# Kernel optimization log

Hardware: AMD Instinct MI355X
Metric: run time of the kernel (lower is better)

## Reference

```python
import jax, jax.numpy as jnp
import numpy as np

L, B, D = 2048, 8, 1024
EPS = 1e-5


def setup_inputs() -> dict:
    key = jax.random.key(0)
    k1, k2 = jax.random.split(key)
    x = jax.random.normal(k1, (L, B, D), dtype=jnp.float32)
    c = jnp.zeros((B, D), dtype=jnp.float32)
    # w_ufr: Linear(D, 3D); weight init normal(std=0.001), bias zero except
    # the reset-gate third which is filled with 2.0 (per the torch init).
    W = jax.random.normal(k2, (3 * D, D), dtype=jnp.float32) * 0.001
    b = jnp.zeros((3 * D,), dtype=jnp.float32).at[2 * D:].set(2.0)
    gamma = jnp.ones((D,), dtype=jnp.float32)
    beta = jnp.zeros((D,), dtype=jnp.float32)
    return {"x": x, "c": c, "W": W, "b": b, "gamma": gamma, "beta": beta}


def _layernorm(x, gamma, beta):
    mu = jnp.mean(x, axis=-1, keepdims=True)
    var = jnp.var(x, axis=-1, keepdims=True)
    return (x - mu) * jax.lax.rsqrt(var + EPS) * gamma + beta


def reference(x, c, W, b, gamma, beta):
    residual = x
    x_norm = _layernorm(x, gamma, beta)            # [L,B,D]
    ufr = jnp.einsum('lbd,ed->lbe', x_norm, W) + b  # [L,B,3D]
    u, f, r = jnp.split(ufr, 3, axis=-1)
    f_gate = jax.nn.sigmoid(f)
    r_gate = jax.nn.sigmoid(r)

    def step(c_prev, fu):
        f_t, u_t = fu
        c_t = f_t * c_prev + (1.0 - f_t) * u_t
        return c_t, c_t

    last_c, c_stack = jax.lax.scan(step, c, (f_gate, u))  # c_stack: [L,B,D]
    hs = r_gate * jnp.tanh(c_stack) + (1.0 - r_gate) * x_norm
    # dropout is identity in eval mode
    return residual + hs, last_c
```

## Files before the change

### kernel.cpp

```cpp
#include <hip/hip_runtime.h>
#include <hip/hip_bf16.h>

#define L_DIM 2048
#define B_DIM 8
#define D_DIM 1024
#define M_DIM (L_DIM * B_DIM)
#define N_DIM (3 * D_DIM)
#define K_DIM D_DIM
#define BD (B_DIM * D_DIM)
#define NCHUNK 64
#define CLEN (L_DIM / NCHUNK)

typedef __attribute__((ext_vector_type(8))) __bf16 bf16x8;
typedef __attribute__((ext_vector_type(4))) __bf16 bf16x4;
typedef __attribute__((ext_vector_type(4))) float f32x4;

#define GLOAD_LDS16(g, l)                                        \
  __builtin_amdgcn_global_load_lds(                              \
      (const __attribute__((address_space(1))) void*)(g),        \
      (__attribute__((address_space(3))) void*)(l), 16, 0, 0)

__device__ __forceinline__ float sigmoidf_(float v) {
  return 1.0f / (1.0f + __expf(-v));
}

__global__ __launch_bounds__(256) void ln_kernel(
    const float* __restrict__ x, const float* __restrict__ gamma,
    const float* __restrict__ beta, __bf16* __restrict__ xn) {
  const int row = blockIdx.x;
  const int tid = threadIdx.x;
  const float4 v = ((const float4*)(x + (size_t)row * D_DIM))[tid];
  float s  = v.x + v.y + v.z + v.w;
  float ss = v.x * v.x + v.y * v.y + v.z * v.z + v.w * v.w;
  #pragma unroll
  for (int off = 32; off > 0; off >>= 1) {
    s  += __shfl_xor(s, off);
    ss += __shfl_xor(ss, off);
  }
  __shared__ float sb[8];
  const int wid = tid >> 6, lane = tid & 63;
  if (lane == 0) { sb[wid] = s; sb[4 + wid] = ss; }
  __syncthreads();
  const float tot  = sb[0] + sb[1] + sb[2] + sb[3];
  const float tot2 = sb[4] + sb[5] + sb[6] + sb[7];
  const float mu  = tot * (1.0f / D_DIM);
  const float var = tot2 * (1.0f / D_DIM) - mu * mu;
  const float rstd = rsqrtf(var + 1e-5f);
  const float4 g  = ((const float4*)gamma)[tid];
  const float4 bt = ((const float4*)beta)[tid];
  bf16x4 o;
  o[0] = (__bf16)((v.x - mu) * rstd * g.x + bt.x);
  o[1] = (__bf16)((v.y - mu) * rstd * g.y + bt.y);
  o[2] = (__bf16)((v.z - mu) * rstd * g.z + bt.z);
  o[3] = (__bf16)((v.w - mu) * rstd * g.w + bt.w);
  ((bf16x4*)(xn + (size_t)row * D_DIM))[tid] = o;
}

__global__ __launch_bounds__(256) void wconv_kernel(
    const float* __restrict__ W, __bf16* __restrict__ Wb) {
  const size_t i = ((size_t)blockIdx.x * 256 + threadIdx.x) * 4;
  const float4 v = *(const float4*)(W + i);
  bf16x4 o;
  o[0] = (__bf16)v.x; o[1] = (__bf16)v.y; o[2] = (__bf16)v.z; o[3] = (__bf16)v.w;
  *(bf16x4*)(Wb + i) = o;
}

__global__ __launch_bounds__(256) void gemm_kernel(
    const __bf16* __restrict__ A,
    const __bf16* __restrict__ Bm,
    const float* __restrict__ bias,
    __bf16* __restrict__ U, __bf16* __restrict__ FG, __bf16* __restrict__ RG) {
  __shared__ __bf16 As[128 * 64];
  __shared__ __bf16 Bs[128 * 64];
  const int tid = threadIdx.x;
  const int lane = tid & 63;
  const int wid = tid >> 6;
  const int wm = wid >> 1, wn = wid & 1;
  const int bm = blockIdx.x, bn = blockIdx.y;

  f32x4 acc[4][4] = {};

  const __bf16* Agbase = A + (size_t)(bm * 128) * K_DIM;
  const __bf16* Bgbase = Bm + (size_t)(bn * 128) * K_DIM;

  for (int kt = 0; kt < K_DIM / 64; ++kt) {
    __syncthreads();
    #pragma unroll
    for (int it = 0; it < 4; ++it) {
      const int ci = it * 256 + tid;
      const int row = ci >> 3, c8 = ci & 7;
      const size_t goff = (size_t)row * K_DIM + kt * 64 + c8 * 8;
      GLOAD_LDS16(Agbase + goff, As + (size_t)ci * 8);
      GLOAD_LDS16(Bgbase + goff, Bs + (size_t)ci * 8);
    }
    __syncthreads();
    #pragma unroll
    for (int ks = 0; ks < 2; ++ks) {
      const int kof = ks * 32 + (lane >> 4) * 8;
      bf16x8 af[4], bf[4];
      #pragma unroll
      for (int fm = 0; fm < 4; ++fm) {
        const int r = wm * 64 + fm * 16 + (lane & 15);
        af[fm] = *(const bf16x8*)(As + r * 64 + kof);
      }
      #pragma unroll
      for (int fn = 0; fn < 4; ++fn) {
        const int r = wn * 64 + fn * 16 + (lane & 15);
        bf[fn] = *(const bf16x8*)(Bs + r * 64 + kof);
      }
      #pragma unroll
      for (int fm = 0; fm < 4; ++fm)
        #pragma unroll
        for (int fn = 0; fn < 4; ++fn)
          acc[fm][fn] = __builtin_amdgcn_mfma_f32_16x16x32_bf16(
              af[fm], bf[fn], acc[fm][fn], 0, 0, 0);
    }
  }

  const int seg = (bn * 128) >> 10;
  const int nbase = (bn * 128) & 1023;
  __bf16* outb = (seg == 0) ? U : ((seg == 1) ? FG : RG);
  const int ccol = lane & 15;
  const int crow = (lane >> 4) * 4;
  #pragma unroll
  for (int fm = 0; fm < 4; ++fm) {
    #pragma unroll
    for (int fn = 0; fn < 4; ++fn) {
      const int ng = bn * 128 + wn * 64 + fn * 16 + ccol;
      const float bv = bias[ng];
      const int nl = nbase + wn * 64 + fn * 16 + ccol;
      const int m0 = bm * 128 + wm * 64 + fm * 16 + crow;
      #pragma unroll
      for (int j = 0; j < 4; ++j) {
        float v = acc[fm][fn][j] + bv;
        if (seg != 0) v = sigmoidf_(v);
        outb[(size_t)(m0 + j) * D_DIM + nl] = (__bf16)v;
      }
    }
  }
}

__global__ __launch_bounds__(256) void scanA_kernel(
    const __bf16* __restrict__ fg, const __bf16* __restrict__ u,
    float* __restrict__ av) {
  const int ci = blockIdx.x;
  const int bd = blockIdx.y * 256 + threadIdx.x;
  float a = 1.0f, v = 0.0f;
  const size_t base = (size_t)ci * CLEN * BD + bd;
  #pragma unroll 8
  for (int i = 0; i < CLEN; ++i) {
    const size_t idx = base + (size_t)i * BD;
    const float f = (float)fg[idx];
    const float uu = (float)u[idx];
    a *= f;
    v = f * v + (1.0f - f) * uu;
  }
  av[(size_t)ci * BD + bd] = a;
  av[(size_t)NCHUNK * BD + (size_t)ci * BD + bd] = v;
}

__global__ __launch_bounds__(256) void scanB_kernel(
    const float* __restrict__ av, const float* __restrict__ c0,
    float* __restrict__ carries, float* __restrict__ out1) {
  const int bd = blockIdx.x * 256 + threadIdx.x;
  float c = c0[bd];
  #pragma unroll 8
  for (int ci = 0; ci < NCHUNK; ++ci) {
    carries[(size_t)ci * BD + bd] = c;
    c = av[(size_t)ci * BD + bd] * c + av[(size_t)NCHUNK * BD + (size_t)ci * BD + bd];
  }
  out1[bd] = c;
}

__global__ __launch_bounds__(256) void scanC_kernel(
    const __bf16* __restrict__ fg, const __bf16* __restrict__ u,
    const __bf16* __restrict__ rg, const __bf16* __restrict__ xn,
    const float* __restrict__ x, const float* __restrict__ carries,
    float* __restrict__ out0) {
  const int ci = blockIdx.x;
  const int bd = blockIdx.y * 256 + threadIdx.x;
  float c = carries[(size_t)ci * BD + bd];
  const size_t base = (size_t)ci * CLEN * BD + bd;
  #pragma unroll 4
  for (int i = 0; i < CLEN; ++i) {
    const size_t idx = base + (size_t)i * BD;
    const float f = (float)fg[idx];
    const float uu = (float)u[idx];
    c = f * c + (1.0f - f) * uu;
    const float r = (float)rg[idx];
    const float xnv = (float)xn[idx];
    const float hs = r * tanhf(c) + (1.0f - r) * xnv;
    out0[idx] = x[idx] + hs;
  }
}

extern "C" void kernel_launch(void* const* d_in, const int* in_sizes, int n_in,
                              void* d_out, int out_size, void* d_ws,
                              size_t ws_size, hipStream_t stream) {
  const float* x     = (const float*)d_in[0];
  const float* c0    = (const float*)d_in[1];
  const float* W     = (const float*)d_in[2];
  const float* bias  = (const float*)d_in[3];
  const float* gamma = (const float*)d_in[4];
  const float* beta  = (const float*)d_in[5];

  float* out0 = (float*)d_out;
  float* out1 = out0 + (size_t)M_DIM * D_DIM;

  char* ws = (char*)d_ws;
  __bf16* xn = (__bf16*)(ws + 0);
  __bf16* Wb = (__bf16*)(ws + 33554432);
  __bf16* U  = (__bf16*)(ws + 39845888);
  __bf16* FG = (__bf16*)(ws + 73400320);
  __bf16* RG = (__bf16*)(ws + 106954752);
  float* av      = (float*)(ws + 140509184);
  float* carries = (float*)(ws + 144703488);

  ln_kernel<<<M_DIM, 256, 0, stream>>>(x, gamma, beta, xn);
  wconv_kernel<<<(N_DIM * K_DIM / 4) / 256, 256, 0, stream>>>(W, Wb);
  gemm_kernel<<<dim3(M_DIM / 128, N_DIM / 128), 256, 0, stream>>>(
      xn, Wb, bias, U, FG, RG);
  scanA_kernel<<<dim3(NCHUNK, BD / 256), 256, 0, stream>>>(FG, U, av);
  scanB_kernel<<<BD / 256, 256, 0, stream>>>(av, c0, carries, out1);
  scanC_kernel<<<dim3(NCHUNK, BD / 256), 256, 0, stream>>>(
      FG, U, RG, xn, x, carries, out0);
}
```

Baseline: 258.8 us.

## Replace GEMM with 256x256-tile double-buffered pipelined MFMA kernel

Replaces the 128x128 single-buffered GEMM with a 512-thread kernel computing 256x256 tiles. It double-buffers LDS with direct global-to-LDS loads interleaved between MFMA phases, using vmcnt waits, barriers and setprio. It also remaps block IDs in an XCD-aware order to improve L2 reuse. The aim is to hide global load latency behind matrix work and raise arithmetic intensity, at the cost of 128KB LDS per block and fragile hand-tuned wait counts.

New measurement: 241.6 us. -6.7%, faster.

```diff
diff --git a/kernel.cpp b/kernel.cpp
--- a/kernel.cpp
+++ b/kernel.cpp
@@ -65,76 +65,150 @@
   *(bf16x4*)(Wb + i) = o;
 }
 
-__global__ __launch_bounds__(256) void gemm_kernel(
+#define VMCNT(n) asm volatile("s_waitcnt vmcnt(" #n ")" ::: "memory")
+
+__global__ __launch_bounds__(512, 2) void gemm256_kernel(
     const __bf16* __restrict__ A,
     const __bf16* __restrict__ Bm,
     const float* __restrict__ bias,
     __bf16* __restrict__ U, __bf16* __restrict__ FG, __bf16* __restrict__ RG) {
-  __shared__ __bf16 As[128 * 64];
-  __shared__ __bf16 Bs[128 * 64];
+  __shared__ __bf16 lds[65536];
   const int tid = threadIdx.x;
   const int lane = tid & 63;
   const int wid = tid >> 6;
-  const int wm = wid >> 1, wn = wid & 1;
-  const int bm = blockIdx.x, bn = blockIdx.y;
-
-  f32x4 acc[4][4] = {};
-
-  const __bf16* Agbase = A + (size_t)(bm * 128) * K_DIM;
-  const __bf16* Bgbase = Bm + (size_t)(bn * 128) * K_DIM;
-
-  for (int kt = 0; kt < K_DIM / 64; ++kt) {
-    __syncthreads();
-    #pragma unroll
-    for (int it = 0; it < 4; ++it) {
-      const int ci = it * 256 + tid;
-      const int row = ci >> 3, c8 = ci & 7;
-      const size_t goff = (size_t)row * K_DIM + kt * 64 + c8 * 8;
-      GLOAD_LDS16(Agbase + goff, As + (size_t)ci * 8);
-      GLOAD_LDS16(Bgbase + goff, Bs + (size_t)ci * 8);
-    }
-    __syncthreads();
-    #pragma unroll
-    for (int ks = 0; ks < 2; ++ks) {
-      const int kof = ks * 32 + (lane >> 4) * 8;
-      bf16x8 af[4], bf[4];
-      #pragma unroll
-      for (int fm = 0; fm < 4; ++fm) {
-        const int r = wm * 64 + fm * 16 + (lane & 15);
-        af[fm] = *(const bf16x8*)(As + r * 64 + kof);
-      }
-      #pragma unroll
-      for (int fn = 0; fn < 4; ++fn) {
-        const int r = wn * 64 + fn * 16 + (lane & 15);
-        bf[fn] = *(const bf16x8*)(Bs + r * 64 + kof);
-      }
-      #pragma unroll
-      for (int fm = 0; fm < 4; ++fm)
-        #pragma unroll
-        for (int fn = 0; fn < 4; ++fn)
-          acc[fm][fn] = __builtin_amdgcn_mfma_f32_16x16x32_bf16(
-              af[fm], bf[fn], acc[fm][fn], 0, 0, 0);
-    }
-  }
-
-  const int seg = (bn * 128) >> 10;
-  const int nbase = (bn * 128) & 1023;
+  const int wm = wid >> 2;
+  const int wn = wid & 3;
+  const int g  = wn >> 1;
+
+  const int bid0 = blockIdx.x;
+  const int bid = (bid0 & 7) * 96 + (bid0 >> 3);
+  const int bm = bid / 12, bn = bid % 12;
+
+  const int arow0 = bm * 256 + wm * 128;
+  const int brow0 = bn * 256 + g * 128;
+  const int akg = wn;
+  const int bkg = wm * 2 + (wn & 1);
+
+#define AUNIT(buf, half, ks) ((buf) * 32768 + (half) * 8192 + (ks) * 4096)
+#define BUNIT(buf, gg, ks)   ((buf) * 32768 + 16384 + (gg) * 8192 + (ks) * 4096)
+
+  auto stageA = [&](int kt2, int ks) {
+    const int buf = kt2 & 1;
+    const __bf16* gs = A + (size_t)arow0 * K_DIM + kt2 * 64 + ks * 32 + akg * 8;
+    __bf16* ls = lds + AUNIT(buf, wm, ks) + akg * 1024;
+    GLOAD_LDS16(gs + (size_t)lane * K_DIM, ls + lane * 8);
+    GLOAD_LDS16(gs + (size_t)(lane + 64) * K_DIM, ls + (lane + 64) * 8);
+  };
+  auto stageB = [&](int kt2, int ks) {
+    const int buf = kt2 & 1;
+    const __bf16* gs = Bm + (size_t)brow0 * K_DIM + kt2 * 64 + ks * 32 + bkg * 8;
+    __bf16* ls = lds + BUNIT(buf, g, ks) + bkg * 1024;
+    GLOAD_LDS16(gs + (size_t)lane * K_DIM, ls + lane * 8);
+    GLOAD_LDS16(gs + (size_t)(lane + 64) * K_DIM, ls + (lane + 64) * 8);
+  };
+
+  const int fr = lane & 15, fk = lane >> 4;
+  auto rdA = [&](int buf, int ks, int m) {
+    return *(const bf16x8*)(lds + AUNIT(buf, wm, ks) + fk * 1024 +
+                            (m * 16 + fr) * 8);
+  };
+  auto rdB = [&](int buf, int ks, int n) {
+    return *(const bf16x8*)(lds + BUNIT(buf, g, ks) + fk * 1024 +
+                            ((wn & 1) * 64 + n * 16 + fr) * 8);
+  };
+
+  f32x4 acc[8][4] = {};
+
+  stageA(0, 0); stageB(0, 0); stageA(0, 1); stageB(0, 1);
+  stageA(1, 0); stageB(1, 0);
+  VMCNT(4);
+  __builtin_amdgcn_s_barrier();
+
+  #pragma unroll 1
+  for (int kt = 0; kt < 16; ++kt) {
+    const int buf = kt & 1;
+    bf16x8 a[4], b[4];
+
+    #pragma unroll
+    for (int m = 0; m < 4; ++m) a[m] = rdA(buf, 0, m);
+    #pragma unroll
+    for (int n = 0; n < 4; ++n) b[n] = rdB(buf, 0, n);
+    if (kt < 15) stageA(kt + 1, 1);
+    __builtin_amdgcn_s_barrier();
+    __builtin_amdgcn_s_setprio(1);
+    #pragma unroll
+    for (int m = 0; m < 4; ++m)
+      #pragma unroll
+      for (int n = 0; n < 4; ++n)
+        acc[m][n] = __builtin_amdgcn_mfma_f32_16x16x32_bf16(a[m], b[n],
+                                                            acc[m][n], 0, 0, 0);
+    __builtin_amdgcn_s_setprio(0);
+    __builtin_amdgcn_s_barrier();
+
+    #pragma unroll
+    for (int m = 0; m < 4; ++m) a[m] = rdA(buf, 0, m + 4);
+    if (kt < 15) stageB(kt + 1, 1);
+    __builtin_amdgcn_s_barrier();
+    __builtin_amdgcn_s_setprio(1);
+    #pragma unroll
+    for (int m = 0; m < 4; ++m)
+      #pragma unroll
+      for (int n = 0; n < 4; ++n)
+        acc[m + 4][n] = __builtin_amdgcn_mfma_f32_16x16x32_bf16(
+            a[m], b[n], acc[m + 4][n], 0, 0, 0);
+    __builtin_amdgcn_s_setprio(0);
+    if (kt == 15) { VMCNT(0); } else { VMCNT(8); }
+    __builtin_amdgcn_s_barrier();
+
+    #pragma unroll
+    for (int m = 0; m < 4; ++m) a[m] = rdA(buf, 1, m);
+    #pragma unroll
+    for (int n = 0; n < 4; ++n) b[n] = rdB(buf, 1, n);
+    if (kt < 14) stageA(kt + 2, 0);
+    __builtin_amdgcn_s_barrier();
+    __builtin_amdgcn_s_setprio(1);
+    #pragma unroll
+    for (int m = 0; m < 4; ++m)
+      #pragma unroll
+      for (int n = 0; n < 4; ++n)
+        acc[m][n] = __builtin_amdgcn_mfma_f32_16x16x32_bf16(a[m], b[n],
+                                                            acc[m][n], 0, 0, 0);
+    __builtin_amdgcn_s_setprio(0);
+    __builtin_amdgcn_s_barrier();
+
+    #pragma unroll
+    for (int m = 0; m < 4; ++m) a[m] = rdA(buf, 1, m + 4);
+    if (kt < 14) stageB(kt + 2, 0);
+    __builtin_amdgcn_s_barrier();
+    __builtin_amdgcn_s_setprio(1);
+    #pragma unroll
+    for (int m = 0; m < 4; ++m)
+      #pragma unroll
+      for (int n = 0; n < 4; ++n)
+        acc[m + 4][n] = __builtin_amdgcn_mfma_f32_16x16x32_bf16(
+            a[m], b[n], acc[m + 4][n], 0, 0, 0);
+    __builtin_amdgcn_s_setprio(0);
+    if (kt < 14) { VMCNT(8); }
+    else if (kt == 14) { VMCNT(4); }
+    __builtin_amdgcn_s_barrier();
+  }
+
+  const int seg = bn >> 2;
   __bf16* outb = (seg == 0) ? U : ((seg == 1) ? FG : RG);
-  const int ccol = lane & 15;
-  const int crow = (lane >> 4) * 4;
+  const int nl0 = (bn & 3) * 256 + wn * 64;
+  const int m00 = bm * 256 + wm * 128;
   #pragma unroll
-  for (int fm = 0; fm < 4; ++fm) {
-    #pragma unroll
-    for (int fn = 0; fn < 4; ++fn) {
-      const int ng = bn * 128 + wn * 64 + fn * 16 + ccol;
-      const float bv = bias[ng];
-      const int nl = nbase + wn * 64 + fn * 16 + ccol;
-      const int m0 = bm * 128 + wm * 64 + fm * 16 + crow;
+  for (int n = 0; n < 4; ++n) {
+    const int col = nl0 + n * 16 + fr;
+    const float bv = bias[seg * 1024 + col];
+    #pragma unroll
+    for (int m = 0; m < 8; ++m) {
+      const int r0 = m00 + m * 16 + fk * 4;
       #pragma unroll
       for (int j = 0; j < 4; ++j) {
-        float v = acc[fm][fn][j] + bv;
+        float v = acc[m][n][j] + bv;
         if (seg != 0) v = sigmoidf_(v);
-        outb[(size_t)(m0 + j) * D_DIM + nl] = (__bf16)v;
+        outb[(size_t)(r0 + j) * D_DIM + col] = (__bf16)v;
       }
     }
   }
@@ -218,7 +292,7 @@
 
   ln_kernel<<<M_DIM, 256, 0, stream>>>(x, gamma, beta, xn);
   wconv_kernel<<<(N_DIM * K_DIM / 4) / 256, 256, 0, stream>>>(W, Wb);
-  gemm_kernel<<<dim3(M_DIM / 128, N_DIM / 128), 256, 0, stream>>>(
+  gemm256_kernel<<<(M_DIM / 256) * (N_DIM / 256), 512, 0, stream>>>(
       xn, Wb, bias, U, FG, RG);
   scanA_kernel<<<dim3(NCHUNK, BD / 256), 256, 0, stream>>>(FG, U, av);
   scanB_kernel<<<BD / 256, 256, 0, stream>>>(av, c0, carries, out1);
```
